# Performance work log

Measured on AMD Instinct MI355X. Metric: run time of the kernel, lower is better.

## Reference

```python
import jax, jax.numpy as jnp
import numpy as np

H = 256  # num_hidden

def setup_inputs() -> dict:
    key = jax.random.key(0)
    k1, k2, k3 = jax.random.split(key, 3)
    B, S, V = 256, 512, 128
    tokens = jax.random.randint(k1, (B, S), 0, V, dtype=jnp.int32)
    emb = jax.random.normal(k2, (V, H), dtype=jnp.float32)
    # Fused gate weights for the four Linear(2H -> H) layers: order [i, f, o, u]
    W = jax.random.normal(k3, (2 * H, 4 * H), dtype=jnp.float32) * (1.0 / np.sqrt(2 * H))
    b = jnp.zeros((4 * H,), dtype=jnp.float32)
    return {"tokens": tokens, "emb": emb, "W": W, "b": b}

def reference(tokens, emb, W, b):
    # tokens: [B, S] int; emb: [V, H]; W: [2H, 4H]; b: [4H]
    x = emb[tokens]                      # [B, S, H] gathered embeddings
    B = x.shape[0]
    h0 = jnp.zeros((B, H), dtype=x.dtype)
    c0 = jnp.zeros((B, H), dtype=x.dtype)

    def step(carry, xt):
        h, c = carry
        z = jnp.concatenate([h, xt], axis=-1) @ W + b   # [B, 4H]
        i = jax.nn.sigmoid(z[:, 0 * H:1 * H])           # 'data' gate
        f = jax.nn.sigmoid(z[:, 1 * H:2 * H])           # 'forget' gate
        o = jax.nn.sigmoid(z[:, 2 * H:3 * H])           # 'output' gate
        u = jnp.tanh(z[:, 3 * H:4 * H])                 # 'input' candidate
        c_new = i * u + f * c
        h_new = o * jnp.tanh(c_new)
        return (h_new, c_new), h_new

    (_, _), hs = jax.lax.scan(step, (h0, c0), jnp.swapaxes(x, 0, 1))  # hs: [S, B, H]
    return jnp.swapaxes(hs, 0, 1)  # [B, S, H]
```

## Files before the change

### kernel.cpp

```cpp
#include <hip/hip_runtime.h>
#include <hip/hip_bf16.h>


#define HID    256
#define FOURH  1024
#define SLEN   512
#define NBATCH 256
#define NVOCAB 128
#define BSZ    16

typedef __attribute__((ext_vector_type(8))) __bf16 bf16x8;
typedef __attribute__((ext_vector_type(4))) float  f32x4;

__device__ __forceinline__ unsigned short f2bf(float x) {
  unsigned int u = __builtin_bit_cast(unsigned int, x);
  u = (u + 0x7FFFu + ((u >> 16) & 1u)) >> 16;
  return (unsigned short)u;
}
__device__ __forceinline__ float sigmoid_(float x) {
  return __builtin_amdgcn_rcpf(1.f + __expf(-x));
}
__device__ __forceinline__ float tanh_(float x) {
  return 1.f - 2.f * __builtin_amdgcn_rcpf(__expf(2.f * x) + 1.f);
}

__global__ __launch_bounds__(256) void lstm_prep(
    const float* __restrict__ emb, const float* __restrict__ W,
    const float* __restrict__ b, float* __restrict__ zx,
    unsigned short* __restrict__ Wb)
{
  const int blk = blockIdx.x;
  if (blk < NVOCAB) {
    __shared__ float ev[HID];
    const int v = blk;
    for (int i = threadIdx.x; i < HID; i += 256) ev[i] = emb[v * HID + i];
    __syncthreads();
    for (int jj = 0; jj < 4; ++jj) {
      const int col = jj * 256 + threadIdx.x;
      float acc = b[col];
      #pragma unroll 4
      for (int k = 0; k < HID; ++k)
        acc += ev[k] * W[(HID + k) * FOURH + col];
      zx[v * FOURH + col] = acc;
    }
  } else {
    int idx = (blk - NVOCAB) * 256 + threadIdx.x;
    const int c = idx >> 9;
    const int rem = idx & 511;
    const int s = rem >> 6, gg = (rem >> 4) & 3, r = rem & 15;
    const int col = 16 * c + r;
    #pragma unroll
    for (int j = 0; j < 8; ++j) {
      const int k = 32 * s + 8 * gg + j;
      Wb[(((c * 8 + s) * 4 + gg) * 16 + r) * 8 + j] = f2bf(W[k * FOURH + col]);
    }
  }
}

__global__ __launch_bounds__(512, 2) void lstm_seq(
    const int* __restrict__ tokens, const float* __restrict__ zx,
    const unsigned short* __restrict__ Wb, float* __restrict__ out)
{
  __shared__ __align__(16) unsigned short hbuf[2][4096];
  const int tid = threadIdx.x;
  const int w = tid >> 6, l = tid & 63;
  const int g = l >> 4, r = l & 15;
  const int b0 = blockIdx.x * BSZ;
  const int row4 = 4 * g;
  const int cb0 = 2 * w;

  for (int i = tid; i < 2 * 4096; i += 512) ((unsigned short*)hbuf)[i] = 0;
  __syncthreads();

  float cst[2][4];
  #pragma unroll
  for (int cb = 0; cb < 2; ++cb)
    #pragma unroll
    for (int j = 0; j < 4; ++j) cst[cb][j] = 0.f;

  const unsigned short* wlane = Wb + l * 8;

  for (int t = 0; t < SLEN; ++t) {
    const int pp = t & 1;

    int tok[4];
    #pragma unroll
    for (int j = 0; j < 4; ++j)
      tok[j] = tokens[(b0 + row4 + j) * SLEN + t];
    float zxv[2][4][4];
    #pragma unroll
    for (int j = 0; j < 4; ++j) {
      const float* zrow = zx + tok[j] * FOURH + r;
      #pragma unroll
      for (int cb = 0; cb < 2; ++cb) {
        const int col16 = (cb0 + cb) * 16;
        #pragma unroll
        for (int q = 0; q < 4; ++q)
          zxv[cb][q][j] = zrow[q * 256 + col16];
      }
    }

    bf16x8 a[8];
    #pragma unroll
    for (int s = 0; s < 8; ++s)
      a[s] = *reinterpret_cast<const bf16x8*>(&hbuf[pp][(s * 64 + l) * 8]);

    f32x4 acc[2][4];
    bf16x8 bfrag[2][8];
    {
      const unsigned short* wp0 = wlane + (size_t)(16 * 0 + cb0 + 0) * 4096;
      #pragma unroll
      for (int s = 0; s < 8; ++s)
        bfrag[0][s] = *reinterpret_cast<const bf16x8*>(wp0 + s * 512);
    }
    #pragma unroll
    for (int u = 0; u < 8; ++u) {
      const int cb = u & 1, q = u >> 1;
      if (u < 7) {
        const int un = u + 1;
        const unsigned short* wpn =
            wlane + (size_t)(16 * (un >> 1) + cb0 + (un & 1)) * 4096;
        #pragma unroll
        for (int s = 0; s < 8; ++s)
          bfrag[un & 1][s] = *reinterpret_cast<const bf16x8*>(wpn + s * 512);
      }
      f32x4 A = {0.f, 0.f, 0.f, 0.f};
      #pragma unroll
      for (int s = 0; s < 8; ++s)
        A = __builtin_amdgcn_mfma_f32_16x16x32_bf16(a[s], bfrag[u & 1][s], A, 0, 0, 0);
      acc[cb][q] = A;
    }

    #pragma unroll
    for (int cb = 0; cb < 2; ++cb) {
      const int cbi = cb0 + cb;
      const int col = 16 * cbi + r;
      const int s = col >> 5, gg = (col >> 3) & 3, jj = col & 7;
      #pragma unroll
      for (int j = 0; j < 4; ++j) {
        const float zi = acc[cb][0][j] + zxv[cb][0][j];
        const float zf = acc[cb][1][j] + zxv[cb][1][j];
        const float zo = acc[cb][2][j] + zxv[cb][2][j];
        const float zu = acc[cb][3][j] + zxv[cb][3][j];
        const float iv = sigmoid_(zi);
        const float fv = sigmoid_(zf);
        const float ov = sigmoid_(zo);
        const float uv = tanh_(zu);
        const float cn = iv * uv + fv * cst[cb][j];
        cst[cb][j] = cn;
        const float hn = ov * tanh_(cn);
        out[(size_t)(b0 + row4 + j) * (SLEN * HID) + (size_t)t * HID + col] = hn;
        hbuf[pp ^ 1][((s * 4 + gg) * 16 + (row4 + j)) * 8 + jj] = f2bf(hn);
      }
    }
    __syncthreads();
  }
}

extern "C" void kernel_launch(void* const* d_in, const int* in_sizes, int n_in,
                              void* d_out, int out_size, void* d_ws, size_t ws_size,
                              hipStream_t stream) {
  const int*   tokens = (const int*)d_in[0];
  const float* emb    = (const float*)d_in[1];
  const float* W      = (const float*)d_in[2];
  const float* b      = (const float*)d_in[3];
  float* out = (float*)d_out;

  float*          zx = (float*)d_ws;
  unsigned short* Wb = (unsigned short*)((char*)d_ws + 512 * 1024);

  lstm_prep<<<256, 256, 0, stream>>>(emb, W, b, zx, Wb);
  lstm_seq<<<16, 512, 0, stream>>>(tokens, zx, Wb, out);
}
```

Baseline: 4.363 ms.

## Keep recurrent weights resident in registers with 16 waves per block

Moves from 8 waves each handling two column blocks to 16 waves each handling one column block. Each wave now loads its bf16 slice of the recurrent weight matrix into registers once before the time loop, instead of re-reading it from global memory or L2 every timestep. This removes per-step weight traffic from the serial recurrence. The cost is about 128 extra VGPRs per lane for weights and larger blocks, which adds register pressure under the 1024-thread launch bound and could cause spills.

```diff
diff --git a/kernel.cpp b/kernel.cpp
--- a/kernel.cpp
+++ b/kernel.cpp
@@ -5,7 +5,6 @@
 #define HID    256
 #define FOURH  1024
 #define SLEN   512
-#define NBATCH 256
 #define NVOCAB 128
 #define BSZ    16
 
@@ -57,7 +56,7 @@
   }
 }
 
-__global__ __launch_bounds__(512, 2) void lstm_seq(
+__global__ __launch_bounds__(1024, 4) void lstm_seq(
     const int* __restrict__ tokens, const float* __restrict__ zx,
     const unsigned short* __restrict__ Wb, float* __restrict__ out)
 {
@@ -67,18 +66,24 @@
   const int g = l >> 4, r = l & 15;
   const int b0 = blockIdx.x * BSZ;
   const int row4 = 4 * g;
-  const int cb0 = 2 * w;
 
-  for (int i = tid; i < 2 * 4096; i += 512) ((unsigned short*)hbuf)[i] = 0;
+  for (int i = tid; i < 2 * 4096; i += 1024) ((unsigned short*)hbuf)[i] = 0;
+
+  bf16x8 wf[32];
+  const unsigned short* wl = Wb + (size_t)l * 8;
+  #pragma unroll
+  for (int q = 0; q < 4; ++q)
+    #pragma unroll
+    for (int s = 0; s < 8; ++s)
+      wf[q * 8 + s] = *reinterpret_cast<const bf16x8*>(
+          wl + (size_t)(16 * q + w) * 4096 + s * 512);
+
+  float cst[4] = {0.f, 0.f, 0.f, 0.f};
+
+  const int colw = 16 * w + r;
+  const int s4 = colw >> 5, gg = (colw >> 3) & 3, jj = colw & 7;
+
   __syncthreads();
-
-  float cst[2][4];
-  #pragma unroll
-  for (int cb = 0; cb < 2; ++cb)
-    #pragma unroll
-    for (int j = 0; j < 4; ++j) cst[cb][j] = 0.f;
-
-  const unsigned short* wlane = Wb + l * 8;
 
   for (int t = 0; t < SLEN; ++t) {
     const int pp = t & 1;
@@ -87,17 +92,12 @@
     #pragma unroll
     for (int j = 0; j < 4; ++j)
       tok[j] = tokens[(b0 + row4 + j) * SLEN + t];
-    float zxv[2][4][4];
+    float zxv[4][4];
     #pragma unroll
     for (int j = 0; j < 4; ++j) {
-      const float* zrow = zx + tok[j] * FOURH + r;
+      const float* zp = zx + (size_t)tok[j] * FOURH + colw;
       #pragma unroll
-      for (int cb = 0; cb < 2; ++cb) {
-        const int col16 = (cb0 + cb) * 16;
-        #pragma unroll
-        for (int q = 0; q < 4; ++q)
-          zxv[cb][q][j] = zrow[q * 256 + col16];
-      }
+      for (int q = 0; q < 4; ++q) zxv[q][j] = zp[q * 256];
     }
 
     bf16x8 a[8];
@@ -105,53 +105,31 @@
     for (int s = 0; s < 8; ++s)
       a[s] = *reinterpret_cast<const bf16x8*>(&hbuf[pp][(s * 64 + l) * 8]);
 
-    f32x4 acc[2][4];
-    bf16x8 bfrag[2][8];
-    {
-      const unsigned short* wp0 = wlane + (size_t)(16 * 0 + cb0 + 0) * 4096;
-      #pragma unroll
-      for (int s = 0; s < 8; ++s)
-        bfrag[0][s] = *reinterpret_cast<const bf16x8*>(wp0 + s * 512);
-    }
+    f32x4 acc[4];
     #pragma unroll
-    for (int u = 0; u < 8; ++u) {
-      const int cb = u & 1, q = u >> 1;
-      if (u < 7) {
-        const int un = u + 1;
-        const unsigned short* wpn =
-            wlane + (size_t)(16 * (un >> 1) + cb0 + (un & 1)) * 4096;
-        #pragma unroll
-        for (int s = 0; s < 8; ++s)
-          bfrag[un & 1][s] = *reinterpret_cast<const bf16x8*>(wpn + s * 512);
-      }
+    for (int q = 0; q < 4; ++q) {
       f32x4 A = {0.f, 0.f, 0.f, 0.f};
       #pragma unroll
       for (int s = 0; s < 8; ++s)
-        A = __builtin_amdgcn_mfma_f32_16x16x32_bf16(a[s], bfrag[u & 1][s], A, 0, 0, 0);
-      acc[cb][q] = A;
+        A = __builtin_amdgcn_mfma_f32_16x16x32_bf16(a[s], wf[q * 8 + s], A, 0, 0, 0);
+      acc[q] = A;
     }
 
     #pragma unroll
-    for (int cb = 0; cb < 2; ++cb) {
-      const int cbi = cb0 + cb;
-      const int col = 16 * cbi + r;
-      const int s = col >> 5, gg = (col >> 3) & 3, jj = col & 7;
-      #pragma unroll
-      for (int j = 0; j < 4; ++j) {
-        const float zi = acc[cb][0][j] + zxv[cb][0][j];
-        const float zf = acc[cb][1][j] + zxv[cb][1][j];
-        const float zo = acc[cb][2][j] + zxv[cb][2][j];
-        const float zu = acc[cb][3][j] + zxv[cb][3][j];
-        const float iv = sigmoid_(zi);
-        const float fv = sigmoid_(zf);
-        const float ov = sigmoid_(zo);
-        const float uv = tanh_(zu);
-        const float cn = iv * uv + fv * cst[cb][j];
-        cst[cb][j] = cn;
-        const float hn = ov * tanh_(cn);
-        out[(size_t)(b0 + row4 + j) * (SLEN * HID) + (size_t)t * HID + col] = hn;
-        hbuf[pp ^ 1][((s * 4 + gg) * 16 + (row4 + j)) * 8 + jj] = f2bf(hn);
-      }
+    for (int j = 0; j < 4; ++j) {
+      const float zi = acc[0][j] + zxv[0][j];
+      const float zf = acc[1][j] + zxv[1][j];
+      const float zo = acc[2][j] + zxv[2][j];
+      const float zu = acc[3][j] + zxv[3][j];
+      const float iv = sigmoid_(zi);
+      const float fv = sigmoid_(zf);
+      const float ov = sigmoid_(zo);
+      const float uv = tanh_(zu);
+      const float cn = iv * uv + fv * cst[j];
+      cst[j] = cn;
+      const float hn = ov * tanh_(cn);
+      out[(size_t)(b0 + row4 + j) * (SLEN * HID) + (size_t)t * HID + colw] = hn;
+      hbuf[pp ^ 1][((s4 * 4 + gg) * 16 + (row4 + j)) * 8 + jj] = f2bf(hn);
     }
     __syncthreads();
   }
@@ -170,5 +148,5 @@
   unsigned short* Wb = (unsigned short*)((char*)d_ws + 512 * 1024);
 
   lstm_prep<<<256, 256, 0, stream>>>(emb, W, b, zx, Wb);
-  lstm_seq<<<16, 512, 0, stream>>>(tokens, zx, Wb, out);
+  lstm_seq<<<16, 1024, 0, stream>>>(tokens, zx, Wb, out);
 }
```

Result: faster. 3.700 ms (-15.2%).
